# Kernel tuning notes

Measured on AMD Instinct MI355X. Metric: run time of the kernel, lower is better.

The kernel has to match this reference:

```python
import jax, jax.numpy as jnp
import numpy as np


def setup_inputs() -> dict:
    key = jax.random.key(0)
    k1, k2 = jax.random.split(key)
    BATCH, SLOTS = 64, 65536   # 64 ciphertexts, 2^16 CKKS slots each
    NUM_T = 16                 # number of BSGS diagonal transforms (shifts 2^0..2^15)
    x = jax.random.normal(k1, (BATCH, SLOTS), dtype=jnp.float32)
    diagonals = jax.random.normal(k2, (NUM_T, SLOTS), dtype=jnp.float32)
    return {"x": x, "diagonals": diagonals, "stride": 1, "reps": 1}


def reference(x, diagonals, stride, reps):
    """FHE BSGS conv-as-linear-transform: rotate / plaintext-multiply / accumulate.

    Mirrors LinearTransform.evaluate_transforms:
      for i: out += roll(x, -2**i * stride) * diagonals[i]
      (two rescales are scale-management no-ops numerically)
      final conv roll by slots // (2 * reps).
    """
    slots = x.shape[-1]
    num_t = diagonals.shape[0]
    # Vectorize the rotations: gather all shifted copies at once.
    # shift for transform i is -2**i * stride (roll left by 2**i*stride).
    shifts = (2 ** jnp.arange(num_t, dtype=jnp.int32)) * stride        # [T]
    base = jnp.arange(slots, dtype=jnp.int32)                          # [S]
    idx = (base[None, :] + shifts[:, None]) % slots                    # [T, S] roll(-s) gather
    rolled = x[:, idx]                                                 # [B, T, S]
    out = jnp.einsum('bts,ts->bs', rolled, diagonals)                  # accumulate products
    # final conv roll: roll(slots // (2*reps)) => shift right
    out = jnp.roll(out, slots // (2 * reps), axis=-1)
    return out
```

## Files before the change

kernel.cpp:

```cpp
#include <hip/hip_runtime.h>


#define SLOTS 65536
#define MASK  65535
#define NB    4

__global__ __launch_bounds__(256) void bsgs_kernel(
    const float* __restrict__ x,
    const float* __restrict__ diag,
    float* __restrict__ out)
{
    const int bid  = blockIdx.x;
    const int y    = bid & 15;
    const int xidx = bid >> 4;
    const int j    = xidx * 1024 + threadIdx.x * 4;
    const int bg   = y * NB;

    const float* __restrict__ xb = x + (size_t)bg * SLOTS;

    float4 acc[NB];
#pragma unroll
    for (int b = 0; b < NB; ++b) acc[b] = make_float4(0.f, 0.f, 0.f, 0.f);

    {
        const float4 d0 = *(const float4*)(diag + 0 * SLOTS + j);
        const float4 d1 = *(const float4*)(diag + 1 * SLOTS + j);
        const float4 d2 = *(const float4*)(diag + 2 * SLOTS + j);
#pragma unroll
        for (int b = 0; b < NB; ++b) {
            const float* xr = xb + (size_t)b * SLOTS;
            const float4 vA = *(const float4*)(xr + j);
            const float4 vB = *(const float4*)(xr + ((j + 4) & MASK));
            acc[b].x += vA.y * d0.x + vA.z * d1.x + vB.x * d2.x;
            acc[b].y += vA.z * d0.y + vA.w * d1.y + vB.y * d2.y;
            acc[b].z += vA.w * d0.z + vB.x * d1.z + vB.z * d2.z;
            acc[b].w += vB.x * d0.w + vB.y * d1.w + vB.w * d2.w;
        }
    }

#pragma unroll
    for (int t = 3; t < 16; ++t) {
        const float4 d = *(const float4*)(diag + t * SLOTS + j);
        const int o = (j + (1 << t)) & MASK;
#pragma unroll
        for (int b = 0; b < NB; ++b) {
            const float4 v = *(const float4*)(xb + (size_t)b * SLOTS + o);
            acc[b].x += v.x * d.x; acc[b].y += v.y * d.y;
            acc[b].z += v.z * d.z; acc[b].w += v.w * d.w;
        }
    }

#pragma unroll
    for (int b = 0; b < NB; ++b)
        *(float4*)(out + (size_t)(bg + b) * SLOTS + (j ^ 32768)) = acc[b];
}

extern "C" void kernel_launch(void* const* d_in, const int* in_sizes, int n_in,
                              void* d_out, int out_size, void* d_ws, size_t ws_size,
                              hipStream_t stream) {
    const float* x    = (const float*)d_in[0];
    const float* diag = (const float*)d_in[1];
    float* out        = (float*)d_out;

    bsgs_kernel<<<dim3(1024), dim3(256), 0, stream>>>(x, diag, out);
}
```

Baseline: 86.38 us.

## Use wavefront shuffles for small rotations and cache diagonals in registers

Loads all 16 diagonal float4s into registers once and reorganizes the loop to process one batch row at a time. For shifts 4 through 128, the rotated x values are now built with cross-lane shuffles of two loaded float4s instead of separate global loads. This cuts global or L2 load instructions per row from about 14 to 9. In exchange it adds 48 shuffles per row and holds 64 extra VGPRs for the diagonals, which may lower occupancy.

```diff
diff --git a/kernel.cpp b/kernel.cpp
--- a/kernel.cpp
+++ b/kernel.cpp
@@ -4,6 +4,11 @@
 #define SLOTS 65536
 #define MASK  65535
 #define NB    4
+
+__device__ __forceinline__ float4 shfl4(const float4 v, int lsel) {
+    return make_float4(__shfl(v.x, lsel, 64), __shfl(v.y, lsel, 64),
+                       __shfl(v.z, lsel, 64), __shfl(v.w, lsel, 64));
+}
 
 __global__ __launch_bounds__(256) void bsgs_kernel(
     const float* __restrict__ x,
@@ -15,38 +20,59 @@
     const int xidx = bid >> 4;
     const int j    = xidx * 1024 + threadIdx.x * 4;
     const int bg   = y * NB;
+    const int lane = threadIdx.x & 63;
 
-    const float* __restrict__ xb = x + (size_t)bg * SLOTS;
+    float4 dreg[16];
+#pragma unroll
+    for (int t = 0; t < 16; ++t)
+        dreg[t] = *(const float4*)(diag + t * SLOTS + j);
 
     float4 acc[NB];
 #pragma unroll
     for (int b = 0; b < NB; ++b) acc[b] = make_float4(0.f, 0.f, 0.f, 0.f);
 
-    {
-        const float4 d0 = *(const float4*)(diag + 0 * SLOTS + j);
-        const float4 d1 = *(const float4*)(diag + 1 * SLOTS + j);
-        const float4 d2 = *(const float4*)(diag + 2 * SLOTS + j);
 #pragma unroll
-        for (int b = 0; b < NB; ++b) {
-            const float* xr = xb + (size_t)b * SLOTS;
-            const float4 vA = *(const float4*)(xr + j);
-            const float4 vB = *(const float4*)(xr + ((j + 4) & MASK));
-            acc[b].x += vA.y * d0.x + vA.z * d1.x + vB.x * d2.x;
-            acc[b].y += vA.z * d0.y + vA.w * d1.y + vB.y * d2.y;
-            acc[b].z += vA.w * d0.z + vB.x * d1.z + vB.z * d2.z;
-            acc[b].w += vB.x * d0.w + vB.y * d1.w + vB.w * d2.w;
+    for (int b = 0; b < NB; ++b) {
+        const float* __restrict__ xr = x + (size_t)(bg + b) * SLOTS;
+
+        const float4 vA = *(const float4*)(xr + j);
+        const float4 vE = *(const float4*)(xr + ((j + 256) & MASK));
+        float4 vd[7];
+#pragma unroll
+        for (int t = 9; t < 16; ++t)
+            vd[t - 9] = *(const float4*)(xr + ((j + (1 << t)) & MASK));
+
+        float4 w[6];
+#pragma unroll
+        for (int i = 0; i < 6; ++i) {
+            const int k  = 1 << i;
+            const int lp = lane + k;
+            const int ls = lp & 63;
+            const float4 a = shfl4(vA, ls);
+            const float4 e = shfl4(vE, ls);
+            const bool useA = lp < 64;
+            w[i] = make_float4(useA ? a.x : e.x, useA ? a.y : e.y,
+                               useA ? a.z : e.z, useA ? a.w : e.w);
         }
-    }
+
+        acc[b].x += vA.y   * dreg[0].x + vA.z   * dreg[1].x;
+        acc[b].y += vA.z   * dreg[0].y + vA.w   * dreg[1].y;
+        acc[b].z += vA.w   * dreg[0].z + w[0].x * dreg[1].z;
+        acc[b].w += w[0].x * dreg[0].w + w[0].y * dreg[1].w;
 
 #pragma unroll
-    for (int t = 3; t < 16; ++t) {
-        const float4 d = *(const float4*)(diag + t * SLOTS + j);
-        const int o = (j + (1 << t)) & MASK;
+        for (int t = 2; t <= 7; ++t) {
+            const float4 v = w[t - 2];
+            acc[b].x += v.x * dreg[t].x; acc[b].y += v.y * dreg[t].y;
+            acc[b].z += v.z * dreg[t].z; acc[b].w += v.w * dreg[t].w;
+        }
+        acc[b].x += vE.x * dreg[8].x; acc[b].y += vE.y * dreg[8].y;
+        acc[b].z += vE.z * dreg[8].z; acc[b].w += vE.w * dreg[8].w;
 #pragma unroll
-        for (int b = 0; b < NB; ++b) {
-            const float4 v = *(const float4*)(xb + (size_t)b * SLOTS + o);
-            acc[b].x += v.x * d.x; acc[b].y += v.y * d.y;
-            acc[b].z += v.z * d.z; acc[b].w += v.w * d.w;
+        for (int t = 9; t < 16; ++t) {
+            const float4 v = vd[t - 9];
+            acc[b].x += v.x * dreg[t].x; acc[b].y += v.y * dreg[t].y;
+            acc[b].z += v.z * dreg[t].z; acc[b].w += v.w * dreg[t].w;
         }
     }
 
```

New measurement: 84.72 us (median of 2 runs). Within noise of the previous version (-1.9%).
